# Performance work log

Measured on AMD Instinct MI355X. Metric: run time of the kernel, lower is better.

## Reference

```python
import jax, jax.numpy as jnp
import numpy as np

T = 256   # time steps
F = 64    # features per step
H = 32    # LSTM hidden size
FORGET_BIAS = 1.0  # TF LSTMCell default


def setup_inputs() -> dict:
    key = jax.random.key(0)
    k1, k2, k3 = jax.random.split(key, 3)
    B = 16384
    x = jax.random.normal(k1, (B, T * F), dtype=jnp.float32)
    W_lstm = jax.random.normal(k2, (F + H, 4 * H), dtype=jnp.float32) * 0.1
    b_lstm = jnp.zeros((4 * H,), dtype=jnp.float32)
    W_dense = jax.random.normal(k3, (H, 1), dtype=jnp.float32) * 0.1
    b_dense = jnp.zeros((1,), dtype=jnp.float32)
    return {"x": x, "W_lstm": W_lstm, "b_lstm": b_lstm,
            "W_dense": W_dense, "b_dense": b_dense}


def reference(x, W_lstm, b_lstm, W_dense, b_dense):
    B = x.shape[0]
    # [B, T*F] -> [T, B, F] for scan over time
    xs = x.reshape(B, T, F).transpose(1, 0, 2)

    def step(carry, x_t):
        c, h = carry
        # TF LSTMCell: concat([inputs, h]) @ kernel + bias, gate order i, j, f, o
        gates = jnp.concatenate([x_t, h], axis=-1) @ W_lstm + b_lstm
        i, j, f, o = jnp.split(gates, 4, axis=-1)
        c_new = c * jax.nn.sigmoid(f + FORGET_BIAS) + jax.nn.sigmoid(i) * jnp.tanh(j)
        h_new = jnp.tanh(c_new) * jax.nn.sigmoid(o)
        return (c_new, h_new), None

    c0 = jnp.zeros((B, H), dtype=x.dtype)
    h0 = jnp.zeros((B, H), dtype=x.dtype)
    (c_T, h_T), _ = jax.lax.scan(step, (c0, h0), xs)

    # dense(1) + ELU on the final hidden state, then flatten like predict()
    out = jax.nn.elu(h_T @ W_dense + b_dense)
    return out.reshape(-1)
```

## Files before the change

### kernel.cpp

```cpp
#include <hip/hip_runtime.h>
#include <stdint.h>

#define T_STEPS 256
#define F_IN 64
#define L2E 1.44269504f

typedef __bf16 bf16x8 __attribute__((ext_vector_type(8)));
typedef float f32x4 __attribute__((ext_vector_type(4)));
typedef uint32_t u32;
typedef uint32_t u32x4 __attribute__((ext_vector_type(4)));

#define GLDS16(gp, lp)                                                         \
    __builtin_amdgcn_global_load_lds(                                          \
        (const __attribute__((address_space(1))) unsigned int*)(gp),           \
        (__attribute__((address_space(3))) unsigned int*)(lp), 16, 0, 0)

__device__ __forceinline__ u32 pk2(float lo, float hi) {
    unsigned short a = __builtin_bit_cast(unsigned short, (__bf16)lo);
    unsigned short b = __builtin_bit_cast(unsigned short, (__bf16)hi);
    return (u32)a | ((u32)b << 16);
}

__global__ __launch_bounds__(256, 1)
void lstm_fused(const float* __restrict__ x,
                const float* __restrict__ Wl,
                const float* __restrict__ bl,
                const float* __restrict__ Wd,
                const float* __restrict__ bd,
                float* __restrict__ out)
{
    __shared__ __align__(16) float xlds[4][4][1024];
    const int lane = threadIdx.x & 63;
    const int wid  = threadIdx.x >> 6;
    const int cl   = lane & 15;
    const int g4   = lane >> 4;
    const int rowBase = blockIdx.x * 64 + wid * 16;

    bf16x8 wfrag[3][8];
#pragma unroll
    for (int kc = 0; kc < 3; ++kc) {
#pragma unroll
        for (int gt = 0; gt < 8; ++gt) {
            bf16x8 v;
#pragma unroll
            for (int j = 0; j < 8; ++j)
                v[j] = (__bf16)Wl[(kc * 32 + g4 * 8 + j) * 128 + gt * 16 + cl];
            wfrag[kc][gt] = v;
        }
    }

    float KI[2][4], KJ[2][4], KF[2][4], KO[2][4];
#pragma unroll
    for (int uh = 0; uh < 2; ++uh) {
        f32x4 bi = *(const f32x4*)(bl +   0 + uh * 16 + g4 * 4);
        f32x4 bj = *(const f32x4*)(bl +  32 + uh * 16 + g4 * 4);
        f32x4 bf = *(const f32x4*)(bl +  64 + uh * 16 + g4 * 4);
        f32x4 bo = *(const f32x4*)(bl +  96 + uh * 16 + g4 * 4);
#pragma unroll
        for (int r = 0; r < 4; ++r) {
            KI[uh][r] = -L2E * bi[r];
            KJ[uh][r] =  2.0f * L2E * bj[r];
            KF[uh][r] = -L2E * (bf[r] + 1.0f);
            KO[uh][r] = -L2E * bo[r];
        }
    }
    const f32x4 wdv0 = *(const f32x4*)(Wd + g4 * 4);
    const f32x4 wdv1 = *(const f32x4*)(Wd + 16 + g4 * 4);
    const float bd0 = bd[0];

    const float* gbase = x + (size_t)(rowBase + (lane >> 2)) * (size_t)(T_STEPS * F_IN)
                           + (size_t)(((lane & 3) ^ ((lane >> 3) & 3)) * 4);

    const int swz = (cl >> 1) & 3;
    const int c0  = ((g4 & 1) * 2)     ^ swz;
    const int c1  = ((g4 & 1) * 2 + 1) ^ swz;
    const int kA  = (g4 >> 1) * 256 + cl * 16;
    const int kB  = kA + 512;

    asm volatile("s_waitcnt vmcnt(0)" ::: "memory");
    __builtin_amdgcn_sched_barrier(0);

#pragma unroll
    for (int s = 0; s < 3; ++s) {
        const float* gp = gbase + s * F_IN;
        GLDS16(gp,      &xlds[wid][s][0]);
        GLDS16(gp + 16, &xlds[wid][s][256]);
        GLDS16(gp + 32, &xlds[wid][s][512]);
        GLDS16(gp + 48, &xlds[wid][s][768]);
    }

    const f32x4 z4 = {0.f, 0.f, 0.f, 0.f};
    float c_st[2][4] = {{0.f,0.f,0.f,0.f},{0.f,0.f,0.f,0.f}};
    float hl[2][4]   = {{0.f,0.f,0.f,0.f},{0.f,0.f,0.f,0.f}};
    u32x4 ahw = {0u, 0u, 0u, 0u};

    const int srcA = cl + 32 * (g4 & 1);
    const int srcB = srcA + 16;
    const int sel  = g4 >> 1;

#define STEP(TT, SLOT) do {                                                    \
    const int tpf = ((TT) + 3 < T_STEPS) ? (TT) + 3 : T_STEPS - 1;             \
    const float* gp = gbase + tpf * F_IN;                                      \
    GLDS16(gp,      &xlds[wid][((SLOT)+3)&3][0]);                              \
    GLDS16(gp + 16, &xlds[wid][((SLOT)+3)&3][256]);                            \
    GLDS16(gp + 32, &xlds[wid][((SLOT)+3)&3][512]);                            \
    GLDS16(gp + 48, &xlds[wid][((SLOT)+3)&3][768]);                            \
    asm volatile("s_waitcnt vmcnt(12)" ::: "memory");                          \
    __builtin_amdgcn_sched_barrier(0);                                         \
    const float* sl = &xlds[wid][SLOT][0];                                     \
    f32x4 xr0 = *(const f32x4*)(sl + kA + c0 * 4);                             \
    f32x4 xr1 = *(const f32x4*)(sl + kA + c1 * 4);                             \
    f32x4 xr2 = *(const f32x4*)(sl + kB + c0 * 4);                             \
    f32x4 xr3 = *(const f32x4*)(sl + kB + c1 * 4);                             \
    bf16x8 ax0, ax1;                                                           \
    _Pragma("unroll")                                                          \
    for (int j = 0; j < 4; ++j) {                                              \
        ax0[j]     = (__bf16)xr0[j];                                           \
        ax0[4 + j] = (__bf16)xr1[j];                                           \
        ax1[j]     = (__bf16)xr2[j];                                           \
        ax1[4 + j] = (__bf16)xr3[j];                                           \
    }                                                                          \
    bf16x8 ah = __builtin_bit_cast(bf16x8, ahw);                               \
    f32x4 acc[8];                                                              \
    _Pragma("unroll")                                                          \
    for (int gt = 0; gt < 8; ++gt) {                                           \
        f32x4 a = __builtin_amdgcn_mfma_f32_16x16x32_bf16(wfrag[0][gt], ax0, z4, 0, 0, 0); \
        a = __builtin_amdgcn_mfma_f32_16x16x32_bf16(wfrag[1][gt], ax1, a, 0, 0, 0);        \
        a = __builtin_amdgcn_mfma_f32_16x16x32_bf16(wfrag[2][gt], ah,  a, 0, 0, 0);        \
        acc[gt] = a;                                                           \
    }                                                                          \
    _Pragma("unroll")                                                          \
    for (int uh = 0; uh < 2; ++uh) {                                           \
        _Pragma("unroll")                                                      \
        for (int r = 0; r < 4; ++r) {                                          \
            float gi = acc[uh][r];                                             \
            float gj = acc[2 + uh][r];                                         \
            float gf = acc[4 + uh][r];                                         \
            float go = acc[6 + uh][r];                                         \
            float sf = __builtin_amdgcn_rcpf(1.0f + __builtin_amdgcn_exp2f(__builtin_fmaf(gf, -L2E, KF[uh][r]))); \
            float si = __builtin_amdgcn_rcpf(1.0f + __builtin_amdgcn_exp2f(__builtin_fmaf(gi, -L2E, KI[uh][r]))); \
            float tj = 1.0f - 2.0f * __builtin_amdgcn_rcpf(1.0f + __builtin_amdgcn_exp2f(__builtin_fmaf(gj, 2.0f * L2E, KJ[uh][r]))); \
            float cn = __builtin_fmaf(c_st[uh][r], sf, si * tj);               \
            float tc = 1.0f - 2.0f * __builtin_amdgcn_rcpf(1.0f + __builtin_amdgcn_exp2f(2.0f * L2E * cn)); \
            float so = __builtin_amdgcn_rcpf(1.0f + __builtin_amdgcn_exp2f(__builtin_fmaf(go, -L2E, KO[uh][r]))); \
            float hh = tc * so;                                                \
            c_st[uh][r] = cn;                                                  \
            hl[uh][r] = hh;                                                    \
        }                                                                      \
    }                                                                          \
    u32 P0 = pk2(hl[0][0], hl[0][1]);                                          \
    u32 P1 = pk2(hl[0][2], hl[0][3]);                                          \
    u32 P2 = pk2(hl[1][0], hl[1][1]);                                          \
    u32 P3 = pk2(hl[1][2], hl[1][3]);                                          \
    int A0 = __shfl((int)P0, srcA, 64), A1 = __shfl((int)P1, srcA, 64);        \
    int A2 = __shfl((int)P2, srcA, 64), A3 = __shfl((int)P3, srcA, 64);        \
    int B0 = __shfl((int)P0, srcB, 64), B1 = __shfl((int)P1, srcB, 64);        \
    int B2 = __shfl((int)P2, srcB, 64), B3 = __shfl((int)P3, srcB, 64);        \
    ahw[0] = (u32)(sel ? A2 : A0);                                             \
    ahw[1] = (u32)(sel ? A3 : A1);                                             \
    ahw[2] = (u32)(sel ? B2 : B0);                                             \
    ahw[3] = (u32)(sel ? B3 : B1);                                             \
} while (0)

    for (int t = 0; t < T_STEPS; t += 4) {
        STEP(t,     0);
        STEP(t + 1, 1);
        STEP(t + 2, 2);
        STEP(t + 3, 3);
    }
#undef STEP

    float v = 0.f;
#pragma unroll
    for (int r = 0; r < 4; ++r) {
        v = __builtin_fmaf(hl[0][r], wdv0[r], v);
        v = __builtin_fmaf(hl[1][r], wdv1[r], v);
    }
    v += __shfl_xor(v, 16, 64);
    v += __shfl_xor(v, 32, 64);
    if (lane < 16) {
        float z = v + bd0;
        out[rowBase + lane] = z > 0.f ? z : (__expf(z) - 1.0f);
    }
}

extern "C" void kernel_launch(void* const* d_in, const int* in_sizes, int n_in,
                              void* d_out, int out_size, void* d_ws, size_t ws_size,
                              hipStream_t stream) {
    const float* x  = (const float*)d_in[0];
    const float* Wl = (const float*)d_in[1];
    const float* bl = (const float*)d_in[2];
    const float* Wd = (const float*)d_in[3];
    const float* bd = (const float*)d_in[4];
    float* out = (float*)d_out;

    const int rows = out_size;
    const int grid = (rows + 63) / 64;
    hipLaunchKernelGGL(lstm_fused, dim3(grid), dim3(256), 0, stream,
                       x, Wl, bl, Wd, bd, out);
}
```

Measured before the change: 257.5 us.

## Split LSTM gate work across two waves per 16-row tile with LDS exchange

Each 16-row batch tile is now handled by a 128-thread block of two wavefronts. Each wave computes half of the gate columns (i/j or f/o) with MFMA, exchanges partial gate results and the bf16 hidden state through LDS, and synchronizes with block barriers twice per step. Gate math is algebraically fused (one reciprocal for the sigmoid*tanh product), and MFMA sections get raised wave priority. This cuts the per-wave serial MFMA and transcendental chain on the recurrence critical path, at the cost of two barriers per timestep and four times as many blocks.

```diff
diff --git a/kernel.cpp b/kernel.cpp
--- a/kernel.cpp
+++ b/kernel.cpp
@@ -8,20 +8,20 @@
 typedef __bf16 bf16x8 __attribute__((ext_vector_type(8)));
 typedef float f32x4 __attribute__((ext_vector_type(4)));
 typedef uint32_t u32;
-typedef uint32_t u32x4 __attribute__((ext_vector_type(4)));
+typedef uint32_t u32x2 __attribute__((ext_vector_type(2)));
 
 #define GLDS16(gp, lp)                                                         \
     __builtin_amdgcn_global_load_lds(                                          \
         (const __attribute__((address_space(1))) unsigned int*)(gp),           \
         (__attribute__((address_space(3))) unsigned int*)(lp), 16, 0, 0)
 
-__device__ __forceinline__ u32 pk2(float lo, float hi) {
+static __device__ __forceinline__ u32 pk2(float lo, float hi) {
     unsigned short a = __builtin_bit_cast(unsigned short, (__bf16)lo);
     unsigned short b = __builtin_bit_cast(unsigned short, (__bf16)hi);
     return (u32)a | ((u32)b << 16);
 }
 
-__global__ __launch_bounds__(256, 1)
+__global__ __launch_bounds__(128, 2)
 void lstm_fused(const float* __restrict__ x,
                 const float* __restrict__ Wl,
                 const float* __restrict__ bl,
@@ -29,89 +29,92 @@
                 const float* __restrict__ bd,
                 float* __restrict__ out)
 {
-    __shared__ __align__(16) float xlds[4][4][1024];
+    __shared__ __align__(16) float  xs[4][1024];
+    __shared__ __align__(16) float  PX [64][4];
+    __shared__ __align__(16) float  SQS[64][4];
+    __shared__ __align__(16) float  SQO[64][4];
+    __shared__ __align__(16) __bf16 hf [64][8];
+
     const int lane = threadIdx.x & 63;
     const int wid  = threadIdx.x >> 6;
     const int cl   = lane & 15;
     const int g4   = lane >> 4;
-    const int rowBase = blockIdx.x * 64 + wid * 16;
-
-    bf16x8 wfrag[3][8];
+    const int rowBase = blockIdx.x * 16;
+
+    bf16x8 wfrag[3][4];
 #pragma unroll
     for (int kc = 0; kc < 3; ++kc) {
 #pragma unroll
-        for (int gt = 0; gt < 8; ++gt) {
+        for (int q = 0; q < 4; ++q) {
             bf16x8 v;
 #pragma unroll
             for (int j = 0; j < 8; ++j)
-                v[j] = (__bf16)Wl[(kc * 32 + g4 * 8 + j) * 128 + gt * 16 + cl];
-            wfrag[kc][gt] = v;
+                v[j] = (__bf16)Wl[(kc * 32 + g4 * 8 + j) * 128 + (wid * 4 + q) * 16 + cl];
+            wfrag[kc][q] = v;
         }
     }
 
-    float KI[2][4], KJ[2][4], KF[2][4], KO[2][4];
-#pragma unroll
-    for (int uh = 0; uh < 2; ++uh) {
-        f32x4 bi = *(const f32x4*)(bl +   0 + uh * 16 + g4 * 4);
-        f32x4 bj = *(const f32x4*)(bl +  32 + uh * 16 + g4 * 4);
-        f32x4 bf = *(const f32x4*)(bl +  64 + uh * 16 + g4 * 4);
-        f32x4 bo = *(const f32x4*)(bl +  96 + uh * 16 + g4 * 4);
-#pragma unroll
-        for (int r = 0; r < 4; ++r) {
-            KI[uh][r] = -L2E * bi[r];
-            KJ[uh][r] =  2.0f * L2E * bj[r];
-            KF[uh][r] = -L2E * (bf[r] + 1.0f);
-            KO[uh][r] = -L2E * bo[r];
-        }
-    }
-    const f32x4 wdv0 = *(const f32x4*)(Wd + g4 * 4);
-    const f32x4 wdv1 = *(const f32x4*)(Wd + 16 + g4 * 4);
+    float K0[2][4], K1[2][4];
+    {
+        const float* bb   = bl + wid * 64;
+        const float  addf = wid ? 1.0f : 0.0f;
+        const float  s1   = wid ? -L2E : -2.0f * L2E;
+#pragma unroll
+        for (int uh = 0; uh < 2; ++uh)
+#pragma unroll
+            for (int r = 0; r < 4; ++r) {
+                K0[uh][r] = -L2E * (bb[uh * 16 + g4 * 4 + r] + addf);
+                K1[uh][r] = s1 * bb[32 + uh * 16 + g4 * 4 + r];
+            }
+    }
     const float bd0 = bd[0];
+    const f32x4 wdA = *(const f32x4*)(Wd + g4 * 8);
+    const f32x4 wdB = *(const f32x4*)(Wd + g4 * 8 + 4);
 
     const float* gbase = x + (size_t)(rowBase + (lane >> 2)) * (size_t)(T_STEPS * F_IN)
                            + (size_t)(((lane & 3) ^ ((lane >> 3) & 3)) * 4);
+
+    asm volatile("s_waitcnt vmcnt(0)" ::: "memory");
+    __builtin_amdgcn_sched_barrier(0);
+
+    const int tT = ((lane >> 5) + 2 * wid) * 16 + (lane & 15);
+    const int e0 = 4 * ((lane >> 4) & 1);
+    *reinterpret_cast<u32x2*>(&hf[tT][e0]) = u32x2{0u, 0u};
+
+#pragma unroll
+    for (int s = 0; s < 3; ++s) {
+        const float* gp = gbase + s * F_IN + wid * 32;
+        GLDS16(gp,      &xs[s][wid * 512]);
+        GLDS16(gp + 16, &xs[s][wid * 512 + 256]);
+    }
+
+    asm volatile("s_waitcnt vmcnt(4)" ::: "memory");
+    asm volatile("s_waitcnt lgkmcnt(0)" ::: "memory");
+    __builtin_amdgcn_sched_barrier(0);
+    __builtin_amdgcn_s_barrier();
+    __builtin_amdgcn_sched_barrier(0);
 
     const int swz = (cl >> 1) & 3;
     const int c0  = ((g4 & 1) * 2)     ^ swz;
     const int c1  = ((g4 & 1) * 2 + 1) ^ swz;
     const int kA  = (g4 >> 1) * 256 + cl * 16;
     const int kB  = kA + 512;
-
-    asm volatile("s_waitcnt vmcnt(0)" ::: "memory");
-    __builtin_amdgcn_sched_barrier(0);
-
-#pragma unroll
-    for (int s = 0; s < 3; ++s) {
-        const float* gp = gbase + s * F_IN;
-        GLDS16(gp,      &xlds[wid][s][0]);
-        GLDS16(gp + 16, &xlds[wid][s][256]);
-        GLDS16(gp + 32, &xlds[wid][s][512]);
-        GLDS16(gp + 48, &xlds[wid][s][768]);
-    }
-
     const f32x4 z4 = {0.f, 0.f, 0.f, 0.f};
-    float c_st[2][4] = {{0.f,0.f,0.f,0.f},{0.f,0.f,0.f,0.f}};
-    float hl[2][4]   = {{0.f,0.f,0.f,0.f},{0.f,0.f,0.f,0.f}};
-    u32x4 ahw = {0u, 0u, 0u, 0u};
-
-    const int srcA = cl + 32 * (g4 & 1);
-    const int srcB = srcA + 16;
-    const int sel  = g4 >> 1;
+
+    float c_st[4] = {0.f, 0.f, 0.f, 0.f};
 
 #define STEP(TT, SLOT) do {                                                    \
+                                                        \
     const int tpf = ((TT) + 3 < T_STEPS) ? (TT) + 3 : T_STEPS - 1;             \
-    const float* gp = gbase + tpf * F_IN;                                      \
-    GLDS16(gp,      &xlds[wid][((SLOT)+3)&3][0]);                              \
-    GLDS16(gp + 16, &xlds[wid][((SLOT)+3)&3][256]);                            \
-    GLDS16(gp + 32, &xlds[wid][((SLOT)+3)&3][512]);                            \
-    GLDS16(gp + 48, &xlds[wid][((SLOT)+3)&3][768]);                            \
-    asm volatile("s_waitcnt vmcnt(12)" ::: "memory");                          \
-    __builtin_amdgcn_sched_barrier(0);                                         \
-    const float* sl = &xlds[wid][SLOT][0];                                     \
+    const float* gp = gbase + tpf * F_IN + wid * 32;                           \
+    GLDS16(gp,      &xs[((SLOT)+3)&3][wid * 512]);                             \
+    GLDS16(gp + 16, &xs[((SLOT)+3)&3][wid * 512 + 256]);                       \
+    const float* sl = &xs[SLOT][0];                                            \
     f32x4 xr0 = *(const f32x4*)(sl + kA + c0 * 4);                             \
     f32x4 xr1 = *(const f32x4*)(sl + kA + c1 * 4);                             \
     f32x4 xr2 = *(const f32x4*)(sl + kB + c0 * 4);                             \
     f32x4 xr3 = *(const f32x4*)(sl + kB + c1 * 4);                             \
+    bf16x8 ah = *reinterpret_cast<const bf16x8*>(&hf[lane][0]);                \
     bf16x8 ax0, ax1;                                                           \
     _Pragma("unroll")                                                          \
     for (int j = 0; j < 4; ++j) {                                              \
@@ -120,46 +123,71 @@
         ax1[j]     = (__bf16)xr2[j];                                           \
         ax1[4 + j] = (__bf16)xr3[j];                                           \
     }                                                                          \
-    bf16x8 ah = __builtin_bit_cast(bf16x8, ahw);                               \
-    f32x4 acc[8];                                                              \
+    f32x4 acc[4];                                                              \
+    __builtin_amdgcn_s_setprio(1);                                             \
     _Pragma("unroll")                                                          \
-    for (int gt = 0; gt < 8; ++gt) {                                           \
-        f32x4 a = __builtin_amdgcn_mfma_f32_16x16x32_bf16(wfrag[0][gt], ax0, z4, 0, 0, 0); \
-        a = __builtin_amdgcn_mfma_f32_16x16x32_bf16(wfrag[1][gt], ax1, a, 0, 0, 0);        \
-        a = __builtin_amdgcn_mfma_f32_16x16x32_bf16(wfrag[2][gt], ah,  a, 0, 0, 0);        \
-        acc[gt] = a;                                                           \
-    }                                                                          \
+    for (int q = 0; q < 4; ++q) {                                              \
+        f32x4 a = __builtin_amdgcn_mfma_f32_16x16x32_bf16(wfrag[0][q], ax0, z4, 0, 0, 0); \
+        a = __builtin_amdgcn_mfma_f32_16x16x32_bf16(wfrag[1][q], ax1, a, 0, 0, 0);        \
+        a = __builtin_amdgcn_mfma_f32_16x16x32_bf16(wfrag[2][q], ah,  a, 0, 0, 0);        \
+        acc[q] = a;                                                            \
+    }                                                                          \
+    __builtin_amdgcn_s_setprio(0);                                             \
+    float Pl[2][4], Sl[2][4], Ol[2][4];                                        \
+    if (wid == 0) {                                                            \
+        _Pragma("unroll")                                                      \
+        for (int uh = 0; uh < 2; ++uh)                                         \
+        _Pragma("unroll")                                                      \
+        for (int r = 0; r < 4; ++r) {                                          \
+            float I = __builtin_amdgcn_exp2f(__builtin_fmaf(acc[uh][r],     -L2E,        K0[uh][r])); \
+            float J = __builtin_amdgcn_exp2f(__builtin_fmaf(acc[2 + uh][r], -2.0f * L2E, K1[uh][r])); \
+            float D = __builtin_amdgcn_rcpf((1.0f + I) * (1.0f + J));          \
+            Pl[uh][r] = (1.0f - J) * D;                                        \
+        }                                                                      \
+        *(f32x4*)&PX[lane][0] = f32x4{Pl[1][0], Pl[1][1], Pl[1][2], Pl[1][3]}; \
+    } else {                                                                   \
+        _Pragma("unroll")                                                      \
+        for (int uh = 0; uh < 2; ++uh)                                         \
+        _Pragma("unroll")                                                      \
+        for (int r = 0; r < 4; ++r) {                                          \
+            float Fv = __builtin_amdgcn_exp2f(__builtin_fmaf(acc[uh][r],     -L2E, K0[uh][r])); \
+            Sl[uh][r] = __builtin_amdgcn_rcpf(1.0f + Fv);                      \
+            Ol[uh][r] = __builtin_amdgcn_exp2f(__builtin_fmaf(acc[2 + uh][r], -L2E, K1[uh][r])); \
+        }                                                                      \
+        *(f32x4*)&SQS[lane][0] = f32x4{Sl[0][0], Sl[0][1], Sl[0][2], Sl[0][3]};\
+        *(f32x4*)&SQO[lane][0] = f32x4{Ol[0][0], Ol[0][1], Ol[0][2], Ol[0][3]};\
+    }                                                                          \
+    asm volatile("s_waitcnt lgkmcnt(0)" ::: "memory");                         \
+    __builtin_amdgcn_sched_barrier(0);                                         \
+    __builtin_amdgcn_s_barrier();                                              \
+    __builtin_amdgcn_sched_barrier(0);                                         \
+                                 \
+    f32x4 Pm, Sv, Ov;                                                          \
+    if (wid == 0) {                                                            \
+        Pm = f32x4{Pl[0][0], Pl[0][1], Pl[0][2], Pl[0][3]};                    \
+        Sv = *(const f32x4*)&SQS[lane][0];                                     \
+        Ov = *(const f32x4*)&SQO[lane][0];                                     \
+    } else {                                                                   \
+        Pm = *(const f32x4*)&PX[lane][0];                                      \
+        Sv = f32x4{Sl[1][0], Sl[1][1], Sl[1][2], Sl[1][3]};                    \
+        Ov = f32x4{Ol[1][0], Ol[1][1], Ol[1][2], Ol[1][3]};                    \
+    }                                                                          \
+    float hh[4];                                                               \
     _Pragma("unroll")                                                          \
-    for (int uh = 0; uh < 2; ++uh) {                                           \
-        _Pragma("unroll")                                                      \
-        for (int r = 0; r < 4; ++r) {                                          \
-            float gi = acc[uh][r];                                             \
-            float gj = acc[2 + uh][r];                                         \
-            float gf = acc[4 + uh][r];                                         \
-            float go = acc[6 + uh][r];                                         \
-            float sf = __builtin_amdgcn_rcpf(1.0f + __builtin_amdgcn_exp2f(__builtin_fmaf(gf, -L2E, KF[uh][r]))); \
-            float si = __builtin_amdgcn_rcpf(1.0f + __builtin_amdgcn_exp2f(__builtin_fmaf(gi, -L2E, KI[uh][r]))); \
-            float tj = 1.0f - 2.0f * __builtin_amdgcn_rcpf(1.0f + __builtin_amdgcn_exp2f(__builtin_fmaf(gj, 2.0f * L2E, KJ[uh][r]))); \
-            float cn = __builtin_fmaf(c_st[uh][r], sf, si * tj);               \
-            float tc = 1.0f - 2.0f * __builtin_amdgcn_rcpf(1.0f + __builtin_amdgcn_exp2f(2.0f * L2E * cn)); \
-            float so = __builtin_amdgcn_rcpf(1.0f + __builtin_amdgcn_exp2f(__builtin_fmaf(go, -L2E, KO[uh][r]))); \
-            float hh = tc * so;                                                \
-            c_st[uh][r] = cn;                                                  \
-            hl[uh][r] = hh;                                                    \
-        }                                                                      \
-    }                                                                          \
-    u32 P0 = pk2(hl[0][0], hl[0][1]);                                          \
-    u32 P1 = pk2(hl[0][2], hl[0][3]);                                          \
-    u32 P2 = pk2(hl[1][0], hl[1][1]);                                          \
-    u32 P3 = pk2(hl[1][2], hl[1][3]);                                          \
-    int A0 = __shfl((int)P0, srcA, 64), A1 = __shfl((int)P1, srcA, 64);        \
-    int A2 = __shfl((int)P2, srcA, 64), A3 = __shfl((int)P3, srcA, 64);        \
-    int B0 = __shfl((int)P0, srcB, 64), B1 = __shfl((int)P1, srcB, 64);        \
-    int B2 = __shfl((int)P2, srcB, 64), B3 = __shfl((int)P3, srcB, 64);        \
-    ahw[0] = (u32)(sel ? A2 : A0);                                             \
-    ahw[1] = (u32)(sel ? A3 : A1);                                             \
-    ahw[2] = (u32)(sel ? B2 : B0);                                             \
-    ahw[3] = (u32)(sel ? B3 : B1);                                             \
+    for (int r = 0; r < 4; ++r) {                                              \
+        float cn = __builtin_fmaf(c_st[r], Sv[r], Pm[r]);                      \
+        float C  = __builtin_amdgcn_exp2f(-2.0f * L2E * cn);                   \
+        float dr = __builtin_amdgcn_rcpf((1.0f + C) * (1.0f + Ov[r]));         \
+        hh[r] = (1.0f - C) * dr;                                               \
+        c_st[r] = cn;                                                          \
+    }                                                                          \
+    *reinterpret_cast<u32x2*>(&hf[tT][e0]) =                                   \
+        u32x2{pk2(hh[0], hh[1]), pk2(hh[2], hh[3])};                           \
+    asm volatile("s_waitcnt vmcnt(4)" ::: "memory");                           \
+    asm volatile("s_waitcnt lgkmcnt(0)" ::: "memory");                         \
+    __builtin_amdgcn_sched_barrier(0);                                         \
+    __builtin_amdgcn_s_barrier();                                              \
+    __builtin_amdgcn_sched_barrier(0);                                         \
 } while (0)
 
     for (int t = 0; t < T_STEPS; t += 4) {
@@ -170,17 +198,20 @@
     }
 #undef STEP
 
-    float v = 0.f;
-#pragma unroll
-    for (int r = 0; r < 4; ++r) {
-        v = __builtin_fmaf(hl[0][r], wdv0[r], v);
-        v = __builtin_fmaf(hl[1][r], wdv1[r], v);
-    }
-    v += __shfl_xor(v, 16, 64);
-    v += __shfl_xor(v, 32, 64);
-    if (lane < 16) {
-        float z = v + bd0;
-        out[rowBase + lane] = z > 0.f ? z : (__expf(z) - 1.0f);
+    if (wid == 0) {
+        bf16x8 hfin = *reinterpret_cast<const bf16x8*>(&hf[lane][0]);
+        float v = 0.f;
+#pragma unroll
+        for (int j = 0; j < 4; ++j) {
+            v = __builtin_fmaf((float)hfin[j],     wdA[j], v);
+            v = __builtin_fmaf((float)hfin[4 + j], wdB[j], v);
+        }
+        v += __shfl_xor(v, 16, 64);
+        v += __shfl_xor(v, 32, 64);
+        if (lane < 16) {
+            float z = v + bd0;
+            out[rowBase + lane] = z > 0.f ? z : (__expf(z) - 1.0f);
+        }
     }
 }
 
@@ -195,7 +226,7 @@
     float* out = (float*)d_out;
 
     const int rows = out_size;
-    const int grid = (rows + 63) / 64;
-    hipLaunchKernelGGL(lstm_fused, dim3(grid), dim3(256), 0, stream,
+    const int grid = (rows + 15) / 16;
+    hipLaunchKernelGGL(lstm_fused, dim3(grid), dim3(128), 0, stream,
                        x, Wl, bl, Wd, bd, out);
 }
```

After: 350.7 us. 36.2% more time.
